# Kernel optimization log

Hardware: AMD Instinct MI355X
Metric: run time of the kernel (lower is better)

The kernel has to match this reference:

```python
import jax, jax.numpy as jnp
import numpy as np

M, K, N, GROUP = 64, 4096, 11008, 128
NGROUPS = K // GROUP  # 32


def setup_inputs() -> dict:
    key = jax.random.key(0)
    k1, k2, k3, k4, k5 = jax.random.split(key, 5)
    x = jax.random.normal(k1, (M, K), dtype=jnp.float32)
    # packed int4 weights: 8 nibbles per int32, full 32-bit entropy
    qweight = jax.random.bits(k2, (K // 8, N), dtype=jnp.uint32).astype(jnp.int32)
    qzeros = jax.random.bits(k3, (NGROUPS, N // 8), dtype=jnp.uint32).astype(jnp.int32)
    scales = jax.random.uniform(k4, (NGROUPS, N), dtype=jnp.float32, minval=0.001, maxval=0.02)
    bias = jax.random.normal(k5, (N,), dtype=jnp.float32) * 0.01
    return {"x": x, "qweight": qweight, "qzeros": qzeros, "scales": scales, "bias": bias}


def dequantize(qweight, qzeros, scales):
    shifts = jnp.arange(8, dtype=jnp.int32) * 4  # nibble bit offsets 0..28
    # unpack weights: [K//8, N] -> [K//8, 8, N] -> [NGROUPS, GROUP, N]
    w = (jnp.right_shift(qweight[:, None, :], shifts[None, :, None]) & 15)
    w = w.reshape(-1, GROUP, qweight.shape[1])
    # unpack zeros: [NGROUPS, N//8] -> [NGROUPS, N//8, 8] -> [NGROUPS, 1, N]; GPTQ stores zero-1
    z = (jnp.right_shift(qzeros[:, :, None], shifts[None, None, :]) & 15) + 1
    z = z.reshape(z.shape[0], 1, -1)
    # scale * (q - zero), per group: [NGROUPS, GROUP, N] -> [K, N]
    W = scales[:, None, :] * (w - z).astype(scales.dtype)
    return W.reshape(-1, W.shape[2])


def reference(x, qweight, qzeros, scales, bias):
    W = dequantize(qweight, qzeros, scales)  # [K, N] fp32
    return jnp.matmul(x, W.astype(x.dtype)) + bias
```

## Files before the change

kernel.cpp:

```cpp
#include <hip/hip_runtime.h>
#include <hip/hip_bf16.h>

namespace {

constexpr int MM = 64;
constexpr int KK = 4096;
constexpr int NN = 11008;
constexpr int NZROW = NN / 8;
constexpr int BN = 128;
constexpr int KSPLIT = 8;
constexpr int KSEG = KK / KSPLIT;
constexpr int NTILES = NN / BN;
constexpr int BK = 32;
constexpr int RS = 20;

typedef float f32x4 __attribute__((ext_vector_type(4)));
typedef short s16x8 __attribute__((ext_vector_type(8)));
typedef int   i32x4 __attribute__((ext_vector_type(4)));

__device__ __forceinline__ int pack_bf16(float a, float b) {
  union { __hip_bfloat162 h; int i; } u;
  u.h.x = __float2bfloat16(a);
  u.h.y = __float2bfloat16(b);
  return u.i;
}

__global__ __launch_bounds__(256) void prep_kernel(
    const float* __restrict__ bias, float* __restrict__ out)
{
  const int i = blockIdx.x * 256 + threadIdx.x;
  out[i] = bias[i % NN];
}

__global__ __launch_bounds__(256, 2) void gptq_gemm_kernel(
    const float* __restrict__ x, const int* __restrict__ qw,
    const int* __restrict__ qz, const float* __restrict__ scales,
    float* __restrict__ out)
{
  __shared__ int As[MM * RS];
  __shared__ int Bs[BN * RS];

  const int tid  = threadIdx.x;
  const int wave = tid >> 6;
  const int lane = tid & 63;
  const int c    = lane & 15;
  const int quad = lane >> 4;

  const int ntile  = blockIdx.x % NTILES;
  const int ks     = blockIdx.x / NTILES;
  const int n0     = ntile * BN;
  const int kbase0 = ks * KSEG;

  const int am   = tid >> 2;
  const int aseg = tid & 3;
  const int bu0  = tid >> 7;
  const int bn   = tid & 127;
  const int mrow = wave * 16 + quad * 4;

  f32x4 acc[8];
  #pragma unroll
  for (int t = 0; t < 8; ++t) acc[t] = {0.f, 0.f, 0.f, 0.f};

  for (int chunk = 0; chunk < KSEG / BK; ++chunk) {
    const int kc = kbase0 + chunk * BK;

    const float* xp = x + am * KK + kc + aseg * 8;
    f32x4 f0 = *(const f32x4*)xp;
    f32x4 f1 = *(const f32x4*)(xp + 4);
    i32x4 pa;
    pa.x = pack_bf16(f0.x, f0.y);
    pa.y = pack_bf16(f0.z, f0.w);
    pa.z = pack_bf16(f1.x, f1.y);
    pa.w = pack_bf16(f1.z, f1.w);
    *(i32x4*)&As[am * RS + aseg * 4] = pa;

    const int g = kc >> 7;
    const int N = n0 + bn;
    const float s  = scales[g * NN + N];
    const int  zn  = (qz[g * NZROW + (N >> 3)] >> ((N & 7) * 4)) & 15;
    const float C  = (float)(0x800000 + zn + 1);
    const int r0 = kc >> 3;
    #pragma unroll
    for (int h = 0; h < 2; ++h) {
      const int u = bu0 + 2 * h;
      const int v = qw[(r0 + u) * NN + N];
      float w0 = s * (__int_as_float(((v      ) & 15) | 0x4B000000) - C);
      float w1 = s * (__int_as_float(((v >>  4) & 15) | 0x4B000000) - C);
      float w2 = s * (__int_as_float(((v >>  8) & 15) | 0x4B000000) - C);
      float w3 = s * (__int_as_float(((v >> 12) & 15) | 0x4B000000) - C);
      float w4 = s * (__int_as_float(((v >> 16) & 15) | 0x4B000000) - C);
      float w5 = s * (__int_as_float(((v >> 20) & 15) | 0x4B000000) - C);
      float w6 = s * (__int_as_float(((v >> 24) & 15) | 0x4B000000) - C);
      float w7 = s * (__int_as_float(((v >> 28) & 15) | 0x4B000000) - C);
      i32x4 pb;
      pb.x = pack_bf16(w0, w1);
      pb.y = pack_bf16(w2, w3);
      pb.z = pack_bf16(w4, w5);
      pb.w = pack_bf16(w6, w7);
      *(i32x4*)&Bs[bn * RS + u * 4] = pb;
    }

    __syncthreads();

    const s16x8 af = *(const s16x8*)&As[(wave * 16 + c) * RS + quad * 4];
    #pragma unroll
    for (int t = 0; t < 8; ++t) {
      const s16x8 bfr = *(const s16x8*)&Bs[(t * 16 + c) * RS + quad * 4];
      acc[t] = __builtin_amdgcn_mfma_f32_16x16x32_bf16(af, bfr, acc[t], 0, 0, 0);
    }

    __syncthreads();
  }

  #pragma unroll
  for (int t = 0; t < 8; ++t) {
    const int N = n0 + t * 16 + c;
    atomicAdd(&out[(mrow + 0) * NN + N], acc[t].x);
    atomicAdd(&out[(mrow + 1) * NN + N], acc[t].y);
    atomicAdd(&out[(mrow + 2) * NN + N], acc[t].z);
    atomicAdd(&out[(mrow + 3) * NN + N], acc[t].w);
  }
}

}

extern "C" void kernel_launch(void* const* d_in, const int* in_sizes, int n_in,
                              void* d_out, int out_size, void* d_ws, size_t ws_size,
                              hipStream_t stream) {
  const float* x      = (const float*)d_in[0];
  const int*   qw     = (const int*)d_in[1];
  const int*   qz     = (const int*)d_in[2];
  const float* scales = (const float*)d_in[3];
  const float* bias   = (const float*)d_in[4];
  float* out = (float*)d_out;

  prep_kernel<<<(MM * NN) / 256, 256, 0, stream>>>(bias, out);
  gptq_gemm_kernel<<<NTILES * KSPLIT, 256, 0, stream>>>(x, qw, qz, scales, out);
}
```

Before: 116.1 us.

## Replace split-K atomic GEMM with register-pipelined full-K per-wave kernel

Converts x once into a bf16, K-major transposed global buffer. The main kernel then runs without LDS or barriers: each wave owns 16 output columns over the full K, keeps eight packed weight words in flight, and double-buffers the x fragments and group scales/zeros in registers. Weights become the MFMA A operand and are packed to bf16 by truncation via perm. Bias is added and the result stored directly, which removes the bias-init kernel and the split-K atomics. The cost is a much smaller grid (86 blocks of 512 threads), which may underfill the GPU and lean on per-wave latency hiding. Truncating the weights also slightly changes rounding.

```diff
diff --git a/kernel.cpp b/kernel.cpp
--- a/kernel.cpp
+++ b/kernel.cpp
@@ -7,118 +7,128 @@
 constexpr int KK = 4096;
 constexpr int NN = 11008;
 constexpr int NZROW = NN / 8;
-constexpr int BN = 128;
-constexpr int KSPLIT = 8;
-constexpr int KSEG = KK / KSPLIT;
-constexpr int NTILES = NN / BN;
-constexpr int BK = 32;
-constexpr int RS = 20;
+constexpr int NTILES = NN / 128;
+constexpr int NCHT = KK / 32;
 
 typedef float f32x4 __attribute__((ext_vector_type(4)));
 typedef short s16x8 __attribute__((ext_vector_type(8)));
 typedef int   i32x4 __attribute__((ext_vector_type(4)));
 
-__device__ __forceinline__ int pack_bf16(float a, float b) {
-  union { __hip_bfloat162 h; int i; } u;
-  u.h.x = __float2bfloat16(a);
-  u.h.y = __float2bfloat16(b);
-  return u.i;
+__device__ __forceinline__ int perm_trunc(float even, float odd) {
+  return (int)__builtin_amdgcn_perm(__float_as_uint(odd), __float_as_uint(even), 0x07060302u);
+}
+__device__ __forceinline__ unsigned rne_adj(float f) {
+  unsigned u = __float_as_uint(f);
+  return u + 0x7FFFu + ((u >> 16) & 1u);
+}
+__device__ __forceinline__ int pack_rne(float even, float odd) {
+  return (int)__builtin_amdgcn_perm(rne_adj(odd), rne_adj(even), 0x07060302u);
 }
 
-__global__ __launch_bounds__(256) void prep_kernel(
-    const float* __restrict__ bias, float* __restrict__ out)
+__device__ short g_xT8[KK * MM];
+
+__global__ __launch_bounds__(256) void xt8_kernel(const float* __restrict__ x)
 {
-  const int i = blockIdx.x * 256 + threadIdx.x;
-  out[i] = bias[i % NN];
+  const int m    = blockIdx.x >> 1;
+  const int kblk = (blockIdx.x & 1) * 256 + threadIdx.x;
+  const float* p = x + m * KK + kblk * 8;
+  const f32x4 a = *(const f32x4*)p;
+  const f32x4 b = *(const f32x4*)(p + 4);
+  i32x4 w;
+  w.x = pack_rne(a.x, a.y);
+  w.y = pack_rne(a.z, a.w);
+  w.z = pack_rne(b.x, b.y);
+  w.w = pack_rne(b.z, b.w);
+  *(i32x4*)(g_xT8 + ((size_t)kblk * MM + m) * 8) = w;
 }
 
-__global__ __launch_bounds__(256, 2) void gptq_gemm_kernel(
-    const float* __restrict__ x, const int* __restrict__ qw,
-    const int* __restrict__ qz, const float* __restrict__ scales,
+__global__ __launch_bounds__(512, 2) void gptq_gemm_kernel(
+    const int* __restrict__ qw, const int* __restrict__ qz,
+    const float* __restrict__ scales, const float* __restrict__ bias,
     float* __restrict__ out)
 {
-  __shared__ int As[MM * RS];
-  __shared__ int Bs[BN * RS];
-
   const int tid  = threadIdx.x;
   const int wave = tid >> 6;
   const int lane = tid & 63;
-  const int c    = lane & 15;
+  const int ml   = lane & 15;
   const int quad = lane >> 4;
 
-  const int ntile  = blockIdx.x % NTILES;
-  const int ks     = blockIdx.x / NTILES;
-  const int n0     = ntile * BN;
-  const int kbase0 = ks * KSEG;
+  const int nw0  = blockIdx.x * 128 + wave * 16;
+  const int ncol = nw0 + ml;
 
-  const int am   = tid >> 2;
-  const int aseg = tid & 3;
-  const int bu0  = tid >> 7;
-  const int bn   = tid & 127;
-  const int mrow = wave * 16 + quad * 4;
+  const int*   qwl = qw + (size_t)quad * NN + ncol;
+  const s16x8* xb  = (const s16x8*)g_xT8;
+  const int    bb  = quad * MM + ml;
 
-  f32x4 acc[8];
+  f32x4 acc[4];
   #pragma unroll
-  for (int t = 0; t < 8; ++t) acc[t] = {0.f, 0.f, 0.f, 0.f};
+  for (int i = 0; i < 4; ++i) acc[i] = {0.f, 0.f, 0.f, 0.f};
 
-  for (int chunk = 0; chunk < KSEG / BK; ++chunk) {
-    const int kc = kbase0 + chunk * BK;
+  int   qv[8];
+  s16x8 bf[2][4];
+  float ps[4];
+  int   pzd[4];
 
-    const float* xp = x + am * KK + kc + aseg * 8;
-    f32x4 f0 = *(const f32x4*)xp;
-    f32x4 f1 = *(const f32x4*)(xp + 4);
-    i32x4 pa;
-    pa.x = pack_bf16(f0.x, f0.y);
-    pa.y = pack_bf16(f0.z, f0.w);
-    pa.z = pack_bf16(f1.x, f1.y);
-    pa.w = pack_bf16(f1.z, f1.w);
-    *(i32x4*)&As[am * RS + aseg * 4] = pa;
-
-    const int g = kc >> 7;
-    const int N = n0 + bn;
-    const float s  = scales[g * NN + N];
-    const int  zn  = (qz[g * NZROW + (N >> 3)] >> ((N & 7) * 4)) & 15;
-    const float C  = (float)(0x800000 + zn + 1);
-    const int r0 = kc >> 3;
-    #pragma unroll
-    for (int h = 0; h < 2; ++h) {
-      const int u = bu0 + 2 * h;
-      const int v = qw[(r0 + u) * NN + N];
-      float w0 = s * (__int_as_float(((v      ) & 15) | 0x4B000000) - C);
-      float w1 = s * (__int_as_float(((v >>  4) & 15) | 0x4B000000) - C);
-      float w2 = s * (__int_as_float(((v >>  8) & 15) | 0x4B000000) - C);
-      float w3 = s * (__int_as_float(((v >> 12) & 15) | 0x4B000000) - C);
-      float w4 = s * (__int_as_float(((v >> 16) & 15) | 0x4B000000) - C);
-      float w5 = s * (__int_as_float(((v >> 20) & 15) | 0x4B000000) - C);
-      float w6 = s * (__int_as_float(((v >> 24) & 15) | 0x4B000000) - C);
-      float w7 = s * (__int_as_float(((v >> 28) & 15) | 0x4B000000) - C);
-      i32x4 pb;
-      pb.x = pack_bf16(w0, w1);
-      pb.y = pack_bf16(w2, w3);
-      pb.z = pack_bf16(w4, w5);
-      pb.w = pack_bf16(w6, w7);
-      *(i32x4*)&Bs[bn * RS + u * 4] = pb;
-    }
-
-    __syncthreads();
-
-    const s16x8 af = *(const s16x8*)&As[(wave * 16 + c) * RS + quad * 4];
-    #pragma unroll
-    for (int t = 0; t < 8; ++t) {
-      const s16x8 bfr = *(const s16x8*)&Bs[(t * 16 + c) * RS + quad * 4];
-      acc[t] = __builtin_amdgcn_mfma_f32_16x16x32_bf16(af, bfr, acc[t], 0, 0, 0);
-    }
-
-    __syncthreads();
+  #pragma unroll
+  for (int i = 0; i < 8; ++i) qv[i] = qwl[(size_t)i * 4 * NN];
+  #pragma unroll
+  for (int mt = 0; mt < 4; ++mt) bf[0][mt] = xb[bb + mt * 16];
+  #pragma unroll
+  for (int s = 0; s < 3; ++s) {
+    ps[s]  = scales[(size_t)s * NN + ncol];
+    pzd[s] = qz[(size_t)s * NZROW + (ncol >> 3)];
   }
 
+  auto chunk = [&](int g, bool refillQ, bool pfB, bool pfS) {
+    const int v = qv[g & 7];
+    if (refillQ) qv[g & 7] = qwl[(size_t)(g + 8) * 4 * NN];
+    if (pfB) {
+      #pragma unroll
+      for (int mt = 0; mt < 4; ++mt)
+        bf[(g + 1) & 1][mt] = xb[bb + (size_t)(g + 1) * 4 * MM + mt * 16];
+    }
+    if (pfS) {
+      const int gs3 = (g >> 2) + 3;
+      ps[gs3 & 3]  = scales[(size_t)gs3 * NN + ncol];
+      pzd[gs3 & 3] = qz[(size_t)gs3 * NZROW + (ncol >> 3)];
+    }
+    const int gs = g >> 2;
+    const float s = ps[gs & 3];
+    const float C = (float)(0x800000 + 1)
+                  + (float)((pzd[gs & 3] >> ((ncol & 7) * 4)) & 15);
+    const float w0 = s * (__int_as_float(((v      ) & 15) | 0x4B000000) - C);
+    const float w1 = s * (__int_as_float(((v >>  4) & 15) | 0x4B000000) - C);
+    const float w2 = s * (__int_as_float(((v >>  8) & 15) | 0x4B000000) - C);
+    const float w3 = s * (__int_as_float(((v >> 12) & 15) | 0x4B000000) - C);
+    const float w4 = s * (__int_as_float(((v >> 16) & 15) | 0x4B000000) - C);
+    const float w5 = s * (__int_as_float(((v >> 20) & 15) | 0x4B000000) - C);
+    const float w6 = s * (__int_as_float(((v >> 24) & 15) | 0x4B000000) - C);
+    const float w7 = s * (__int_as_float(((v >> 28) & 15) | 0x4B000000) - C);
+    i32x4 b;
+    b.x = perm_trunc(w0, w1); b.y = perm_trunc(w2, w3);
+    b.z = perm_trunc(w4, w5); b.w = perm_trunc(w6, w7);
+    const s16x8 wf = __builtin_bit_cast(s16x8, b);
+    #pragma unroll
+    for (int mt = 0; mt < 4; ++mt)
+      acc[mt] = __builtin_amdgcn_mfma_f32_16x16x32_bf16(wf, bf[g & 1][mt], acc[mt], 0, 0, 0);
+  };
+
+  for (int base = 0; base < NCHT - 16; base += 16) {
+    #pragma unroll
+    for (int i = 0; i < 16; ++i)
+      chunk(base + i, true, true, (i & 3) == 0);
+  }
   #pragma unroll
-  for (int t = 0; t < 8; ++t) {
-    const int N = n0 + t * 16 + c;
-    atomicAdd(&out[(mrow + 0) * NN + N], acc[t].x);
-    atomicAdd(&out[(mrow + 1) * NN + N], acc[t].y);
-    atomicAdd(&out[(mrow + 2) * NN + N], acc[t].z);
-    atomicAdd(&out[(mrow + 3) * NN + N], acc[t].w);
+  for (int i = 0; i < 16; ++i) {
+    const int g = NCHT - 16 + i;
+    chunk(g, i < 8, i < 15, i == 0);
+  }
+
+  const f32x4 b4 = *(const f32x4*)(bias + nw0 + quad * 4);
+  #pragma unroll
+  for (int mt = 0; mt < 4; ++mt) {
+    const f32x4 r = acc[mt] + b4;
+    *(f32x4*)(out + (size_t)(mt * 16 + ml) * NN + nw0 + quad * 4) = r;
   }
 }
 
@@ -134,6 +144,6 @@
   const float* bias   = (const float*)d_in[4];
   float* out = (float*)d_out;
 
-  prep_kernel<<<(MM * NN) / 256, 256, 0, stream>>>(bias, out);
-  gptq_gemm_kernel<<<NTILES * KSPLIT, 256, 0, stream>>>(x, qw, qz, scales, out);
+  xt8_kernel<<<2 * MM, 256, 0, stream>>>(x);
+  gptq_gemm_kernel<<<NTILES, 512, 0, stream>>>(qw, qz, scales, bias, out);
 }
```

Measured after the change: 126.9 us. +9.3%, slower.
